# Optimization experiments

Measured on AMD Instinct MI355X. Metric: run time of the kernel, lower is better.

## Reference

```python
import jax, jax.numpy as jnp
import numpy as np

# Level grid shapes: (T_i, H_i, W_i, C_i); K=(1,2,2) -> K_prod=4 folded into features
GRID_SIZES = [(120, 9, 16, 64), (60, 9, 16, 128), (30, 9, 16, 256)]
K_PROD = 4
C_OUT = 128
C_SUM = 64 + 128 + 256  # 448
INIT_SCALE = 0.001


def setup_inputs() -> dict:
    key = jax.random.key(0)
    ks = jax.random.split(key, 8)
    N, T, H, W = 2, 12, 36, 64
    inp = {
        'coor_t': jax.random.uniform(ks[0], (N, T), jnp.float32, -1.0, 1.0),
        'coor_h': jax.random.uniform(ks[1], (N, H), jnp.float32, -1.0, 1.0),
        'coor_w': jax.random.uniform(ks[2], (N, W), jnp.float32, -1.0, 1.0),
    }
    for i, (Tg, Hg, Wg, Cg) in enumerate(GRID_SIZES):
        inp[f'g{i}'] = jax.random.normal(ks[3 + i], (Tg * Hg * Wg, K_PROD * Cg), jnp.float32) * INIT_SCALE
    lim = 1.0 / np.sqrt(C_SUM)
    inp['lin_w'] = jax.random.uniform(ks[6], (C_OUT, C_SUM), jnp.float32, -lim, lim)
    inp['lin_b'] = jax.random.uniform(ks[7], (C_OUT,), jnp.float32, -lim, lim)
    return inp


def _prep_axis(c, S):
    # map [-1,1] -> [0, S-1] (align_corners=True), corner indices + frac weight
    x = (c + 1.0) * 0.5 * (S - 1)
    x0 = jnp.clip(jnp.floor(x), 0.0, S - 1)
    i0 = x0.astype(jnp.int32)
    i1 = jnp.clip(i0 + 1, 0, S - 1)
    return i0, i1, x - x0


def _interp3d(grid, coor_t, coor_h, coor_w):
    # grid: [Tg,Hg,Wg,Cf]; coords: [N,T],[N,H],[N,W] in [-1,1] -> [N,T,H,W,Cf]
    Tg, Hg, Wg, Cf = grid.shape
    t0, t1, ft = _prep_axis(coor_t, Tg)
    h0, h1, fh = _prep_axis(coor_h, Hg)
    w0, w1, fw = _prep_axis(coor_w, Wg)

    def g(ti, hi, wi):
        return grid[ti[:, :, None, None], hi[:, None, :, None], wi[:, None, None, :]]

    ft_ = ft[:, :, None, None, None]
    fh_ = fh[:, None, :, None, None]
    fw_ = fw[:, None, None, :, None]
    lo = ((g(t0, h0, w0) * (1 - fw_) + g(t0, h0, w1) * fw_) * (1 - fh_) +
          (g(t0, h1, w0) * (1 - fw_) + g(t0, h1, w1) * fw_) * fh_)
    hi = ((g(t1, h0, w0) * (1 - fw_) + g(t1, h0, w1) * fw_) * (1 - fh_) +
          (g(t1, h1, w0) * (1 - fw_) + g(t1, h1, w1) * fw_) * fh_)
    return lo * (1 - ft_) + hi * ft_


def reference(coor_t, coor_h, coor_w, g0, g1, g2, lin_w, lin_b):
    N, T = coor_t.shape
    H = coor_h.shape[1]
    W = coor_w.shape[1]
    grids = [g0, g1, g2]
    enc = []
    for i, (Tg, Hg, Wg, Cg) in enumerate(GRID_SIZES):
        weight = grids[i].reshape(Tg, Hg, Wg, K_PROD * Cg)
        e = _interp3d(weight, coor_t, coor_h, coor_w)  # [N,T,H,W,K*Cg]
        enc.append(e.reshape(N, T * H * W * K_PROD, Cg))
    feat = jnp.concatenate(enc, axis=-1)  # [N, T*H*W*K, 448]
    out = feat @ lin_w.T + lin_b          # [N, T*H*W*K, 128]
    return out.reshape(N, T, H, W, K_PROD * C_OUT)
```

## Files before the change

### kernel.cpp

```cpp
#include <hip/hip_runtime.h>

typedef __bf16 bf16x8 __attribute__((ext_vector_type(8)));
typedef __bf16 bf16x4 __attribute__((ext_vector_type(4)));
typedef float  f32x4  __attribute__((ext_vector_type(4)));

__device__ __forceinline__ bf16x8 pack8(float4 a, float4 b) {
    bf16x8 r;
    r[0] = (__bf16)a.x; r[1] = (__bf16)a.y; r[2] = (__bf16)a.z; r[3] = (__bf16)a.w;
    r[4] = (__bf16)b.x; r[5] = (__bf16)b.y; r[6] = (__bf16)b.z; r[7] = (__bf16)b.w;
    return r;
}

__global__ __launch_bounds__(256)
void gemmG(const float* __restrict__ g0, const float* __restrict__ g1,
           const float* __restrict__ g2, const float* __restrict__ W,
           const float* __restrict__ coor_t, __bf16* __restrict__ G)
{
    __shared__ __bf16 As[64][40];
    __shared__ __bf16 Bs[128][40];

    const int m0 = blockIdx.x * 64;
    const int nt = m0 / 576;
    const float c = coor_t[nt];

    const int tid  = threadIdx.x;
    const int wid  = tid >> 6;
    const int lane = tid & 63;
    const int lrow = lane & 15;
    const int lk   = (lane >> 4) * 8;

    const int srow = tid >> 2;
    const int q    = tid & 3;
    const int rem  = (m0 % 576) + srow;
    const int hw   = rem >> 2;
    const int kp   = rem & 3;

    const int bcol = tid >> 1;
    const int half = tid & 1;

    f32x4 acc[8];
#pragma unroll
    for (int ct = 0; ct < 8; ct++) acc[ct] = f32x4{0.f, 0.f, 0.f, 0.f};

    for (int k0 = 0; k0 < 448; k0 += 32) {
        const float* gp; int off, Cg, Tg;
        if (k0 < 64)       { gp = g0; off = 0;   Cg = 64;  Tg = 120; }
        else if (k0 < 192) { gp = g1; off = 64;  Cg = 128; Tg = 60;  }
        else               { gp = g2; off = 192; Cg = 256; Tg = 30;  }

        float x  = (c + 1.0f) * 0.5f * (float)(Tg - 1);
        float x0 = fminf(fmaxf(floorf(x), 0.0f), (float)(Tg - 1));
        int   i0 = (int)x0;
        int   i1 = (i0 + 1 < Tg - 1) ? (i0 + 1) : (Tg - 1);
        float ft = x - x0;
        float omf = 1.0f - ft;

        {
            const size_t ch = (size_t)(k0 - off) + q * 8;
            const float4* s0 = (const float4*)(gp + ((size_t)(i0 * 144 + hw) * 4 + kp) * Cg + ch);
            const float4* s1 = (const float4*)(gp + ((size_t)(i1 * 144 + hw) * 4 + kp) * Cg + ch);
            float4 a0 = s0[0], a1 = s0[1];
            float4 b0 = s1[0], b1 = s1[1];
            float4 v0, v1;
            v0.x = a0.x * omf + b0.x * ft; v0.y = a0.y * omf + b0.y * ft;
            v0.z = a0.z * omf + b0.z * ft; v0.w = a0.w * omf + b0.w * ft;
            v1.x = a1.x * omf + b1.x * ft; v1.y = a1.y * omf + b1.y * ft;
            v1.z = a1.z * omf + b1.z * ft; v1.w = a1.w * omf + b1.w * ft;
            *(bf16x8*)&As[srow][q * 8] = pack8(v0, v1);
        }
        {
            const float4* src = (const float4*)(W + (size_t)bcol * 448 + k0 + half * 16);
            float4 f0 = src[0], f1 = src[1], f2 = src[2], f3 = src[3];
            *(bf16x8*)&Bs[bcol][half * 16 + 0] = pack8(f0, f1);
            *(bf16x8*)&Bs[bcol][half * 16 + 8] = pack8(f2, f3);
        }
        __syncthreads();

        bf16x8 a = *(const bf16x8*)&As[wid * 16 + lrow][lk];
        bf16x8 bfrag[8];
#pragma unroll
        for (int ct = 0; ct < 8; ct++)
            bfrag[ct] = *(const bf16x8*)&Bs[ct * 16 + lrow][lk];
#pragma unroll
        for (int ct = 0; ct < 8; ct++)
            acc[ct] = __builtin_amdgcn_mfma_f32_16x16x32_bf16(a, bfrag[ct], acc[ct], 0, 0, 0);
        __syncthreads();
    }

    const int r0 = m0 + wid * 16 + (lane >> 4) * 4;
#pragma unroll
    for (int ct = 0; ct < 8; ct++) {
        const int col = ct * 16 + lrow;
#pragma unroll
        for (int j = 0; j < 4; j++)
            G[(size_t)(r0 + j) * 128 + col] = (__bf16)acc[ct][j];
    }
}

__global__ __launch_bounds__(256)
void finalk(const bf16x4* __restrict__ G, const float* __restrict__ coor_h,
            const float* __restrict__ coor_w, const float* __restrict__ lin_b,
            f32x4* __restrict__ out)
{
    int v   = blockIdx.x * 256 + threadIdx.x;
    int kc4 = v & 127;
    int w   = (v >> 7) & 63;
    int r   = v >> 13;
    int h   = r % 36;
    int nt  = r / 36;
    int n   = nt / 12;

    float ch = coor_h[n * 36 + h];
    float cw = coor_w[n * 64 + w];

    float xh  = (ch + 1.0f) * 0.5f * 8.0f;
    float xh0 = fminf(fmaxf(floorf(xh), 0.0f), 8.0f);
    int   h0  = (int)xh0;
    int   h1  = (h0 + 1 < 8) ? (h0 + 1) : 8;
    float fh  = xh - xh0;
    float xw  = (cw + 1.0f) * 0.5f * 15.0f;
    float xw0 = fminf(fmaxf(floorf(xw), 0.0f), 15.0f);
    int   w0  = (int)xw0;
    int   w1  = (w0 + 1 < 15) ? (w0 + 1) : 15;
    float fw  = xw - xw0;

    int base = nt * 18432 + kc4;
    bf16x4 g00 = G[base + (h0 * 16 + w0) * 128];
    bf16x4 g01 = G[base + (h0 * 16 + w1) * 128];
    bf16x4 g10 = G[base + (h1 * 16 + w0) * 128];
    bf16x4 g11 = G[base + (h1 * 16 + w1) * 128];

    float4 b = ((const float4*)lin_b)[kc4 & 31];
    float ofw = 1.0f - fw, ofh = 1.0f - fh;

    f32x4 o;
    o[0] = ((float)g00[0] * ofw + (float)g01[0] * fw) * ofh + ((float)g10[0] * ofw + (float)g11[0] * fw) * fh + b.x;
    o[1] = ((float)g00[1] * ofw + (float)g01[1] * fw) * ofh + ((float)g10[1] * ofw + (float)g11[1] * fw) * fh + b.y;
    o[2] = ((float)g00[2] * ofw + (float)g01[2] * fw) * ofh + ((float)g10[2] * ofw + (float)g11[2] * fw) * fh + b.z;
    o[3] = ((float)g00[3] * ofw + (float)g01[3] * fw) * ofh + ((float)g10[3] * ofw + (float)g11[3] * fw) * fh + b.w;
    __builtin_nontemporal_store(o, &out[v]);
}

extern "C" void kernel_launch(void* const* d_in, const int* in_sizes, int n_in,
                              void* d_out, int out_size, void* d_ws, size_t ws_size,
                              hipStream_t stream)
{
    const float* coor_t = (const float*)d_in[0];
    const float* coor_h = (const float*)d_in[1];
    const float* coor_w = (const float*)d_in[2];
    const float* g0     = (const float*)d_in[3];
    const float* g1     = (const float*)d_in[4];
    const float* g2     = (const float*)d_in[5];
    const float* lin_w  = (const float*)d_in[6];
    const float* lin_b  = (const float*)d_in[7];

    __bf16* G = (__bf16*)d_ws;

    gemmG<<<216, 256, 0, stream>>>(g0, g1, g2, lin_w, coor_t, G);

    finalk<<<27648, 256, 0, stream>>>((const bf16x4*)G, coor_h, coor_w, lin_b,
                                      (f32x4*)d_out);
}
```

Baseline: 186.0 us.

## Pipeline GEMM K-loop with register prefetch and stage G rows in LDS

```diff
diff --git a/kernel.cpp b/kernel.cpp
--- a/kernel.cpp
+++ b/kernel.cpp
@@ -16,8 +16,8 @@
            const float* __restrict__ g2, const float* __restrict__ W,
            const float* __restrict__ coor_t, __bf16* __restrict__ G)
 {
-    __shared__ __bf16 As[64][40];
-    __shared__ __bf16 Bs[128][40];
+    __shared__ __bf16 As[64][72];
+    __shared__ __bf16 Bs[128][72];
 
     const int m0 = blockIdx.x * 64;
     const int nt = m0 / 576;
@@ -34,57 +34,84 @@
     const int rem  = (m0 % 576) + srow;
     const int hw   = rem >> 2;
     const int kp   = rem & 3;
-
     const int bcol = tid >> 1;
     const int half = tid & 1;
 
+    int i0_0, i1_0, i0_1, i1_1, i0_2, i1_2;
+    float ft_0, ft_1, ft_2;
+    {
+        float x, x0;
+        x = (c + 1.0f) * 0.5f * 119.0f;
+        x0 = fminf(fmaxf(floorf(x), 0.0f), 119.0f);
+        i0_0 = (int)x0; i1_0 = (i0_0 + 1 < 119) ? i0_0 + 1 : 119; ft_0 = x - x0;
+        x = (c + 1.0f) * 0.5f * 59.0f;
+        x0 = fminf(fmaxf(floorf(x), 0.0f), 59.0f);
+        i0_1 = (int)x0; i1_1 = (i0_1 + 1 < 59) ? i0_1 + 1 : 59; ft_1 = x - x0;
+        x = (c + 1.0f) * 0.5f * 29.0f;
+        x0 = fminf(fmaxf(floorf(x), 0.0f), 29.0f);
+        i0_2 = (int)x0; i1_2 = (i0_2 + 1 < 29) ? i0_2 + 1 : 29; ft_2 = x - x0;
+    }
+
     f32x4 acc[8];
 #pragma unroll
     for (int ct = 0; ct < 8; ct++) acc[ct] = f32x4{0.f, 0.f, 0.f, 0.f};
 
-    for (int k0 = 0; k0 < 448; k0 += 32) {
-        const float* gp; int off, Cg, Tg;
-        if (k0 < 64)       { gp = g0; off = 0;   Cg = 64;  Tg = 120; }
-        else if (k0 < 192) { gp = g1; off = 64;  Cg = 128; Tg = 60;  }
-        else               { gp = g2; off = 192; Cg = 256; Tg = 30;  }
-
-        float x  = (c + 1.0f) * 0.5f * (float)(Tg - 1);
-        float x0 = fminf(fmaxf(floorf(x), 0.0f), (float)(Tg - 1));
-        int   i0 = (int)x0;
-        int   i1 = (i0 + 1 < Tg - 1) ? (i0 + 1) : (Tg - 1);
-        float ft = x - x0;
-        float omf = 1.0f - ft;
-
+    float4 ra0[4], ra1[4], rb[8];
+    float  ft_s = 0.f;
+
+    auto load_chunk = [&](int kk) {
+        const int gi = (kk == 0) ? 0 : ((kk < 3) ? 1 : 2);
+        const float* gp = (gi == 0) ? g0 : ((gi == 1) ? g1 : g2);
+        const int off = (gi == 0) ? 0 : ((gi == 1) ? 64 : 192);
+        const int Cg  = (gi == 0) ? 64 : ((gi == 1) ? 128 : 256);
+        const int i0  = (gi == 0) ? i0_0 : ((gi == 1) ? i0_1 : i0_2);
+        const int i1  = (gi == 0) ? i1_0 : ((gi == 1) ? i1_1 : i1_2);
+        ft_s          = (gi == 0) ? ft_0 : ((gi == 1) ? ft_1 : ft_2);
+        const size_t ch = (size_t)(kk * 64 - off) + q * 16;
+        const float4* s0 = (const float4*)(gp + ((size_t)(i0 * 144 + hw) * 4 + kp) * Cg + ch);
+        const float4* s1 = (const float4*)(gp + ((size_t)(i1 * 144 + hw) * 4 + kp) * Cg + ch);
+#pragma unroll
+        for (int j = 0; j < 4; j++) { ra0[j] = s0[j]; ra1[j] = s1[j]; }
+        const float4* sb = (const float4*)(W + (size_t)bcol * 448 + kk * 64 + half * 32);
+#pragma unroll
+        for (int j = 0; j < 8; j++) rb[j] = sb[j];
+    };
+
+    load_chunk(0);
+
+#pragma unroll
+    for (int kc = 0; kc < 7; kc++) {
+        if (kc) __syncthreads();
         {
-            const size_t ch = (size_t)(k0 - off) + q * 8;
-            const float4* s0 = (const float4*)(gp + ((size_t)(i0 * 144 + hw) * 4 + kp) * Cg + ch);
-            const float4* s1 = (const float4*)(gp + ((size_t)(i1 * 144 + hw) * 4 + kp) * Cg + ch);
-            float4 a0 = s0[0], a1 = s0[1];
-            float4 b0 = s1[0], b1 = s1[1];
-            float4 v0, v1;
-            v0.x = a0.x * omf + b0.x * ft; v0.y = a0.y * omf + b0.y * ft;
-            v0.z = a0.z * omf + b0.z * ft; v0.w = a0.w * omf + b0.w * ft;
-            v1.x = a1.x * omf + b1.x * ft; v1.y = a1.y * omf + b1.y * ft;
-            v1.z = a1.z * omf + b1.z * ft; v1.w = a1.w * omf + b1.w * ft;
-            *(bf16x8*)&As[srow][q * 8] = pack8(v0, v1);
-        }
-        {
-            const float4* src = (const float4*)(W + (size_t)bcol * 448 + k0 + half * 16);
-            float4 f0 = src[0], f1 = src[1], f2 = src[2], f3 = src[3];
-            *(bf16x8*)&Bs[bcol][half * 16 + 0] = pack8(f0, f1);
-            *(bf16x8*)&Bs[bcol][half * 16 + 8] = pack8(f2, f3);
+            const float f = ft_s, omf = 1.0f - f;
+            float4 v[4];
+#pragma unroll
+            for (int j = 0; j < 4; j++) {
+                v[j].x = ra0[j].x * omf + ra1[j].x * f;
+                v[j].y = ra0[j].y * omf + ra1[j].y * f;
+                v[j].z = ra0[j].z * omf + ra1[j].z * f;
+                v[j].w = ra0[j].w * omf + ra1[j].w * f;
+            }
+            *(bf16x8*)&As[srow][q * 16 + 0] = pack8(v[0], v[1]);
+            *(bf16x8*)&As[srow][q * 16 + 8] = pack8(v[2], v[3]);
+            *(bf16x8*)&Bs[bcol][half * 32 + 0]  = pack8(rb[0], rb[1]);
+            *(bf16x8*)&Bs[bcol][half * 32 + 8]  = pack8(rb[2], rb[3]);
+            *(bf16x8*)&Bs[bcol][half * 32 + 16] = pack8(rb[4], rb[5]);
+            *(bf16x8*)&Bs[bcol][half * 32 + 24] = pack8(rb[6], rb[7]);
         }
         __syncthreads();
-
-        bf16x8 a = *(const bf16x8*)&As[wid * 16 + lrow][lk];
-        bf16x8 bfrag[8];
-#pragma unroll
-        for (int ct = 0; ct < 8; ct++)
-            bfrag[ct] = *(const bf16x8*)&Bs[ct * 16 + lrow][lk];
-#pragma unroll
-        for (int ct = 0; ct < 8; ct++)
-            acc[ct] = __builtin_amdgcn_mfma_f32_16x16x32_bf16(a, bfrag[ct], acc[ct], 0, 0, 0);
-        __syncthreads();
+        if (kc < 6) load_chunk(kc + 1);
+#pragma unroll
+        for (int sub = 0; sub < 2; sub++) {
+            bf16x8 a = *(const bf16x8*)&As[wid * 16 + lrow][sub * 32 + lk];
+            bf16x8 bfrag[8];
+#pragma unroll
+            for (int ct = 0; ct < 8; ct++)
+                bfrag[ct] = *(const bf16x8*)&Bs[ct * 16 + lrow][sub * 32 + lk];
+#pragma unroll
+            for (int ct = 0; ct < 8; ct++)
+                acc[ct] = __builtin_amdgcn_mfma_f32_16x16x32_bf16(a, bfrag[ct], acc[ct], 0, 0, 0);
+        }
     }
 
     const int r0 = m0 + wid * 16 + (lane >> 4) * 4;
@@ -98,47 +125,68 @@
 }
 
 __global__ __launch_bounds__(256)
-void finalk(const bf16x4* __restrict__ G, const float* __restrict__ coor_h,
+void finalk(const __bf16* __restrict__ G, const float* __restrict__ coor_h,
             const float* __restrict__ coor_w, const float* __restrict__ lin_b,
             f32x4* __restrict__ out)
 {
-    int v   = blockIdx.x * 256 + threadIdx.x;
-    int kc4 = v & 127;
-    int w   = (v >> 7) & 63;
-    int r   = v >> 13;
-    int h   = r % 36;
-    int nt  = r / 36;
-    int n   = nt / 12;
-
-    float ch = coor_h[n * 36 + h];
-    float cw = coor_w[n * 64 + w];
-
-    float xh  = (ch + 1.0f) * 0.5f * 8.0f;
-    float xh0 = fminf(fmaxf(floorf(xh), 0.0f), 8.0f);
-    int   h0  = (int)xh0;
-    int   h1  = (h0 + 1 < 8) ? (h0 + 1) : 8;
-    float fh  = xh - xh0;
-    float xw  = (cw + 1.0f) * 0.5f * 15.0f;
-    float xw0 = fminf(fmaxf(floorf(xw), 0.0f), 15.0f);
-    int   w0  = (int)xw0;
-    int   w1  = (w0 + 1 < 15) ? (w0 + 1) : 15;
-    float fw  = xw - xw0;
-
-    int base = nt * 18432 + kc4;
-    bf16x4 g00 = G[base + (h0 * 16 + w0) * 128];
-    bf16x4 g01 = G[base + (h0 * 16 + w1) * 128];
-    bf16x4 g10 = G[base + (h1 * 16 + w0) * 128];
-    bf16x4 g11 = G[base + (h1 * 16 + w1) * 128];
-
-    float4 b = ((const float4*)lin_b)[kc4 & 31];
-    float ofw = 1.0f - fw, ofh = 1.0f - fh;
-
-    f32x4 o;
-    o[0] = ((float)g00[0] * ofw + (float)g01[0] * fw) * ofh + ((float)g10[0] * ofw + (float)g11[0] * fw) * fh + b.x;
-    o[1] = ((float)g00[1] * ofw + (float)g01[1] * fw) * ofh + ((float)g10[1] * ofw + (float)g11[1] * fw) * fh + b.y;
-    o[2] = ((float)g00[2] * ofw + (float)g01[2] * fw) * ofh + ((float)g10[2] * ofw + (float)g11[2] * fw) * fh + b.z;
-    o[3] = ((float)g00[3] * ofw + (float)g01[3] * fw) * ofh + ((float)g10[3] * ofw + (float)g11[3] * fw) * fh + b.w;
-    __builtin_nontemporal_store(o, &out[v]);
+    __shared__ __bf16 Ls[2][8192];
+
+    const int blk = blockIdx.x;
+    const int h   = blk % 36;
+    const int nt  = blk / 36;
+    const int n   = nt / 12;
+    const int tid = threadIdx.x;
+
+    const float chv = coor_h[n * 36 + h];
+    const float xh  = (chv + 1.0f) * 0.5f * 8.0f;
+    const float xh0 = fminf(fmaxf(floorf(xh), 0.0f), 8.0f);
+    const int   h0  = (int)xh0;
+    const int   h1  = (h0 + 1 < 8) ? h0 + 1 : 8;
+    const float fh  = xh - xh0, ofh = 1.0f - fh;
+
+    {
+        const f32x4* r0 = (const f32x4*)G + (size_t)nt * 9216 + h0 * 1024;
+        const f32x4* r1 = (const f32x4*)G + (size_t)nt * 9216 + h1 * 1024;
+        f32x4* L0 = (f32x4*)&Ls[0][0];
+        f32x4* L1 = (f32x4*)&Ls[1][0];
+#pragma unroll
+        for (int j = 0; j < 4; j++) {
+            L0[j * 256 + tid] = r0[j * 256 + tid];
+            L1[j * 256 + tid] = r1[j * 256 + tid];
+        }
+    }
+    __syncthreads();
+
+    const bf16x4* L0v = (const bf16x4*)&Ls[0][0];
+    const bf16x4* L1v = (const bf16x4*)&Ls[1][0];
+    const size_t obase = (size_t)blk * 8192;
+
+#pragma unroll 4
+    for (int it = 0; it < 32; ++it) {
+        const int idx = it * 256 + tid;
+        const int w   = idx >> 7;
+        const int kc4 = idx & 127;
+
+        const float cwv = coor_w[n * 64 + w];
+        const float xw  = (cwv + 1.0f) * 0.5f * 15.0f;
+        const float xw0 = fminf(fmaxf(floorf(xw), 0.0f), 15.0f);
+        const int   w0  = (int)xw0;
+        const int   w1  = (w0 + 1 < 15) ? w0 + 1 : 15;
+        const float fw  = xw - xw0, ofw = 1.0f - fw;
+
+        const bf16x4 g00 = L0v[w0 * 128 + kc4];
+        const bf16x4 g01 = L0v[w1 * 128 + kc4];
+        const bf16x4 g10 = L1v[w0 * 128 + kc4];
+        const bf16x4 g11 = L1v[w1 * 128 + kc4];
+        const float4 b = ((const float4*)lin_b)[kc4 & 31];
+
+        f32x4 o;
+        o[0] = ((float)g00[0] * ofw + (float)g01[0] * fw) * ofh + ((float)g10[0] * ofw + (float)g11[0] * fw) * fh + b.x;
+        o[1] = ((float)g00[1] * ofw + (float)g01[1] * fw) * ofh + ((float)g10[1] * ofw + (float)g11[1] * fw) * fh + b.y;
+        o[2] = ((float)g00[2] * ofw + (float)g01[2] * fw) * ofh + ((float)g10[2] * ofw + (float)g11[2] * fw) * fh + b.z;
+        o[3] = ((float)g00[3] * ofw + (float)g01[3] * fw) * ofh + ((float)g10[3] * ofw + (float)g11[3] * fw) * fh + b.w;
+        __builtin_nontemporal_store(o, &out[obase + idx]);
+    }
 }
 
 extern "C" void kernel_launch(void* const* d_in, const int* in_sizes, int n_in,
@@ -157,7 +205,5 @@
     __bf16* G = (__bf16*)d_ws;
 
     gemmG<<<216, 256, 0, stream>>>(g0, g1, g2, lin_w, coor_t, G);
-
-    finalk<<<27648, 256, 0, stream>>>((const bf16x4*)G, coor_h, coor_w, lin_b,
-                                      (f32x4*)d_out);
-}
+    finalk<<<864, 256, 0, stream>>>(G, coor_h, coor_w, lin_b, (f32x4*)d_out);
+}
```

After: 185.2 us. Within noise of the previous version (-0.4%).
